# Kernel tuning notes

Hardware: AMD Instinct MI355X
Metric: run time of the kernel (lower is better)

Reference implementation:

```python
import jax, jax.numpy as jnp
import numpy as np

N_NODES = 100000


def gcn_conv(x, src, dst, W, b, n_nodes):
    """PyG GCNConv: add self-loops, symmetric degree normalization, X W, scatter-add."""
    # Linear transform first (small out dim -> cheaper messages)
    h = x @ W  # [N, F_out]
    # Add self-loops
    loop = jnp.arange(n_nodes, dtype=src.dtype)
    s = jnp.concatenate([src, loop])
    d = jnp.concatenate([dst, loop])
    # Degree (in-degree over dst, incl. self-loops), deg^{-1/2}
    deg = jax.ops.segment_sum(jnp.ones_like(d, dtype=h.dtype), d, num_segments=n_nodes)
    dinv = jnp.where(deg > 0, jax.lax.rsqrt(deg), 0.0)
    norm = dinv[s] * dinv[d]  # [E+N]
    # Gather-scale-scatter aggregation
    msgs = h[s] * norm[:, None]  # [E+N, F_out]
    out = jax.ops.segment_sum(msgs, d, num_segments=n_nodes)
    return out + b


def setup_inputs() -> dict:
    key = jax.random.key(0)
    ks = jax.random.split(key, 4)
    n, f_in, f_hid, f_out = N_NODES, 512, 16, 7
    n_edges = 3200000
    x = jax.random.normal(ks[0], (n, f_in), dtype=jnp.float32)
    edge_index = jax.random.randint(ks[1], (2, n_edges), 0, n, dtype=jnp.int64)
    W1 = jax.random.normal(ks[2], (f_in, f_hid), dtype=jnp.float32) / np.sqrt(f_in)
    b1 = jnp.zeros((f_hid,), dtype=jnp.float32)
    W2 = jax.random.normal(ks[3], (f_hid, f_out), dtype=jnp.float32) / np.sqrt(f_hid)
    b2 = jnp.zeros((f_out,), dtype=jnp.float32)
    return {"x": x, "edge_index": edge_index, "W1": W1, "b1": b1, "W2": W2, "b2": b2}


def reference(x, edge_index, W1, b1, W2, b2):
    n = x.shape[0]
    src, dst = edge_index[0], edge_index[1]
    h = gcn_conv(x, src, dst, W1, b1, n)
    h = jax.nn.relu(h)
    out = gcn_conv(h, src, dst, W2, b2, n)
    return out
```

## Files before the change

kernel.cpp:

```cpp
#include <hip/hip_runtime.h>

#define F_IN 512
#define F_HID 16
#define F_OUT 7
#define BUCKET 128
#define LB 7
#define CHUNK 4096
#define MAXNB 1024
#define BSTR 8192
#define BSTR2 8704

#define RPB 256
#define KHALF 256

typedef int   int4v   __attribute__((ext_vector_type(4)));
typedef float float2v __attribute__((ext_vector_type(2)));
typedef float float4v __attribute__((ext_vector_type(4)));
typedef unsigned int uint4v __attribute__((ext_vector_type(4)));

static __device__ __forceinline__ unsigned short f2bf(float f) {
    unsigned int u = __float_as_uint(f);
    u += 0x7FFFu + ((u >> 16) & 1u);
    return (unsigned short)(u >> 16);
}
static __device__ __forceinline__ float bf2f(unsigned short s) {
    return __uint_as_float((unsigned int)s << 16);
}

__global__ void k_init(int* __restrict__ cursor, int NB) {
    int i = blockIdx.x * 256 + threadIdx.x;
    if (i < NB) cursor[i] = i * BSTR;
}

__global__ __launch_bounds__(256) void k_place4(
        const int* __restrict__ src, const int* __restrict__ dst,
        int* __restrict__ cursor, int* __restrict__ bedges, int E, int NB) {
    __shared__ int h[MAXNB];
    __shared__ int s[MAXNB];
    __shared__ int wtot[4];
    __shared__ int sedge[CHUNK];
    __shared__ unsigned short sbkt[CHUNK];
    int t = threadIdx.x, blk = blockIdx.x;
    for (int i = t; i < MAXNB; i += 256) h[i] = 0;
    __syncthreads();
    int base = blk * CHUNK;
    int4v d4[4], s4[4];
#pragma unroll
    for (int it = 0; it < 4; ++it) {
        int e = base + (it * 256 + t) * 4;
        if (e < E) {
            d4[it] = __builtin_nontemporal_load((const int4v*)(dst + e));
            s4[it] = __builtin_nontemporal_load((const int4v*)(src + e));
        } else {
            int sent = NB << LB;
            d4[it].x = sent; d4[it].y = sent; d4[it].z = sent; d4[it].w = sent;
            s4[it].x = 0;    s4[it].y = 0;    s4[it].z = 0;    s4[it].w = 0;
        }
        atomicAdd(&h[d4[it].x >> LB], 1);
        atomicAdd(&h[d4[it].y >> LB], 1);
        atomicAdd(&h[d4[it].z >> LB], 1);
        atomicAdd(&h[d4[it].w >> LB], 1);
    }
    __syncthreads();
    int i0 = t << 2;
    int v0 = h[i0], v1 = h[i0 + 1], v2 = h[i0 + 2], v3 = h[i0 + 3];
    int sum = v0 + v1 + v2 + v3;
    int lane = t & 63, w = t >> 6;
    int sincl = sum;
#pragma unroll
    for (int off = 1; off < 64; off <<= 1) {
        int u = __shfl_up(sincl, off);
        if (lane >= off) sincl += u;
    }
    if (lane == 63) wtot[w] = sincl;
    __syncthreads();
    int wb = 0;
#pragma unroll
    for (int ww = 0; ww < 4; ++ww) if (ww < w) wb += wtot[ww];
    int excl = wb + sincl - sum;
    int pe[4] = {excl, excl + v0, excl + v0 + v1, excl + v0 + v1 + v2};
    int vv[4] = {v0, v1, v2, v3};
#pragma unroll
    for (int j = 0; j < 4; ++j) {
        int i = i0 + j;
        h[i] = pe[j];
        int db = 0;
        if (i < NB && vv[j] > 0)
            db = atomicAdd(&cursor[i], vv[j]) - pe[j];
        s[i] = db;
    }
    __syncthreads();
#pragma unroll
    for (int it = 0; it < 4; ++it) {
        int d, sv, b, p;
        d = d4[it].x; sv = s4[it].x; b = d >> LB; p = atomicAdd(&h[b], 1);
        sedge[p] = (sv << 8) | (d & (BUCKET - 1)); sbkt[p] = (unsigned short)b;
        d = d4[it].y; sv = s4[it].y; b = d >> LB; p = atomicAdd(&h[b], 1);
        sedge[p] = (sv << 8) | (d & (BUCKET - 1)); sbkt[p] = (unsigned short)b;
        d = d4[it].z; sv = s4[it].z; b = d >> LB; p = atomicAdd(&h[b], 1);
        sedge[p] = (sv << 8) | (d & (BUCKET - 1)); sbkt[p] = (unsigned short)b;
        d = d4[it].w; sv = s4[it].w; b = d >> LB; p = atomicAdd(&h[b], 1);
        sedge[p] = (sv << 8) | (d & (BUCKET - 1)); sbkt[p] = (unsigned short)b;
    }
    __syncthreads();
    for (int j = t; j < CHUNK; j += 256) {
        int b = sbkt[j];
        if (b < NB)
            __builtin_nontemporal_store(sedge[j], bedges + s[b] + j);
    }
}

__global__ __launch_bounds__(256) void k_psort(
        const int* __restrict__ cursor, const int* __restrict__ bedges,
        int* __restrict__ bedges2, float* __restrict__ dinv,
        int* __restrict__ node_off, int* __restrict__ node_nq, int n) {
    __shared__ int cnt[BUCKET];
    __shared__ int sc[BUCKET];
    __shared__ int cur[BUCKET];
    __shared__ int sedge[BSTR2];
    int b = blockIdx.x, t = threadIdx.x;
    int base = b * BSTR;
    int ne = cursor[b] - base;
    if (t < BUCKET) cnt[t] = 0;
    __syncthreads();
    int nq = ne >> 2, tail = ne & 3;
    for (int q = t; q < nq; q += 256) {
        int4v v = *(const int4v*)(bedges + base + (q << 2));
        atomicAdd(&cnt[v.x & 127], 1);
        atomicAdd(&cnt[v.y & 127], 1);
        atomicAdd(&cnt[v.z & 127], 1);
        atomicAdd(&cnt[v.w & 127], 1);
    }
    if (t < tail) atomicAdd(&cnt[bedges[base + (nq << 2) + t] & 127], 1);
    __syncthreads();
    int p = 0;
    if (t < BUCKET) { p = (cnt[t] + 3) & ~3; sc[t] = p; }
    __syncthreads();
    for (int off = 1; off < BUCKET; off <<= 1) {
        int v = 0;
        if (t < BUCKET) { v = sc[t]; if (t >= off) v += sc[t - off]; }
        __syncthreads();
        if (t < BUCKET) sc[t] = v;
        __syncthreads();
    }
    if (t < BUCKET) {
        int w = sc[t] - p;
        cur[t] = w;
        int node = b * BUCKET + t;
        if (node < n) {
            dinv[node] = rsqrtf((float)(cnt[t] + 1));
            node_off[node] = b * BSTR2 + w;
            node_nq[node] = p >> 2;
        }
    }
    __syncthreads();
    for (int q = t; q < nq; q += 256) {
        int4v v = *(const int4v*)(bedges + base + (q << 2));
        int pos;
        pos = atomicAdd(&cur[v.x & 127], 1); sedge[pos] = v.x >> 8;
        pos = atomicAdd(&cur[v.y & 127], 1); sedge[pos] = v.y >> 8;
        pos = atomicAdd(&cur[v.z & 127], 1); sedge[pos] = v.z >> 8;
        pos = atomicAdd(&cur[v.w & 127], 1); sedge[pos] = v.w >> 8;
    }
    if (t < tail) {
        int v = bedges[base + (nq << 2) + t];
        int pos = atomicAdd(&cur[v & 127], 1); sedge[pos] = v >> 8;
    }
    __syncthreads();
    if (t < BUCKET) {
        int endc = cur[t];
        for (int i = endc; i < sc[t]; ++i) sedge[i] = n;
    }
    __syncthreads();
    int total = sc[BUCKET - 1];
    int* dst2 = bedges2 + b * BSTR2;
    for (int j4 = t; j4 < (total >> 2); j4 += 256) {
        int4v v = *(const int4v*)(sedge + (j4 << 2));
        __builtin_nontemporal_store(v, (int4v*)(dst2 + (j4 << 2)));
    }
}

__global__ __launch_bounds__(256) void k_gemm1d(
        const float* __restrict__ x, const float* __restrict__ W,
        float* __restrict__ part, int n) {
    int b  = blockIdx.x >> 1;
    int ks = blockIdx.x & 1;
    int r  = b * RPB + threadIdx.x;
    if (r >= n) return;
    const float* xr = x + (size_t)r * F_IN + ks * KHALF;
    const float2v* W2v = (const float2v*)(W + (size_t)ks * KHALF * F_HID);

    float2v acc2[F_HID / 2];
#pragma unroll
    for (int c = 0; c < F_HID / 2; ++c) acc2[c] = (float2v){0.0f, 0.0f};

    for (int k4 = 0; k4 < KHALF / 4; k4 += 8) {
        float4v v[8];
#pragma unroll
        for (int j = 0; j < 8; ++j)
            v[j] = *(const float4v*)(xr + ((k4 + j) << 2));
#pragma unroll
        for (int j = 0; j < 8; ++j) {
            int k = (k4 + j) << 2;
#pragma unroll
            for (int c2 = 0; c2 < F_HID / 2; ++c2) {
                acc2[c2] += v[j].x * W2v[(k + 0) * (F_HID / 2) + c2];
                acc2[c2] += v[j].y * W2v[(k + 1) * (F_HID / 2) + c2];
                acc2[c2] += v[j].z * W2v[(k + 2) * (F_HID / 2) + c2];
                acc2[c2] += v[j].w * W2v[(k + 3) * (F_HID / 2) + c2];
            }
        }
    }
    const float* a = (const float*)acc2;
    float4v* o = (float4v*)(part + ((size_t)ks * n + r) * F_HID);
    float4v w0 = {a[0],  a[1],  a[2],  a[3]};
    float4v w1 = {a[4],  a[5],  a[6],  a[7]};
    float4v w2 = {a[8],  a[9],  a[10], a[11]};
    float4v w3 = {a[12], a[13], a[14], a[15]};
    o[0] = w0; o[1] = w1; o[2] = w2; o[3] = w3;
}

__global__ void k_fin1(const float* __restrict__ part, const float* __restrict__ dinv,
                       unsigned short* __restrict__ h1b, unsigned short* __restrict__ h2b,
                       int n) {
    int tg = blockIdx.x * 256 + threadIdx.x;
    int r = tg >> 4, c = tg & 15;
    if (r > n) return;
    if (r == n) {
        h1b[(size_t)r * F_HID + c] = 0;
        if (c < 8) h2b[((size_t)r << 3) + c] = 0;
        return;
    }
    float v = part[(size_t)r * F_HID + c] + part[((size_t)n + r) * F_HID + c];
    h1b[(size_t)r * F_HID + c] = f2bf(dinv[r] * v);
}

__global__ __launch_bounds__(1024) void k_aggF1(
        const int* __restrict__ node_off, const int* __restrict__ node_nq,
        const int* __restrict__ bedges2, const unsigned short* __restrict__ h1b,
        const float* __restrict__ dinv, const float* __restrict__ b1,
        const float* __restrict__ W2, unsigned short* __restrict__ h2b, int n) {
    int tg = blockIdx.x * 1024 + threadIdx.x;
    int node = tg >> 4, c = tg & 15;
    if (node >= n) return;
    int off = node_off[node], nq = node_nq[node];
    float acc = bf2f(h1b[(size_t)node * F_HID + c]);
    for (int q = 0; q < nq; ++q) {
        int4v s = *(const int4v*)(bedges2 + off + (q << 2));
        float v0 = bf2f(h1b[(size_t)s.x * F_HID + c]);
        float v1 = bf2f(h1b[(size_t)s.y * F_HID + c]);
        float v2 = bf2f(h1b[(size_t)s.z * F_HID + c]);
        float v3 = bf2f(h1b[(size_t)s.w * F_HID + c]);
        acc += v0 + v1 + v2 + v3;
    }
    float dv = dinv[node];
    float z = fmaxf(dv * acc + b1[c], 0.0f);
    float h[F_OUT];
#pragma unroll
    for (int o = 0; o < F_OUT; ++o) h[o] = z * W2[c * F_OUT + o];
#pragma unroll
    for (int sft = 8; sft >= 1; sft >>= 1)
#pragma unroll
        for (int o = 0; o < F_OUT; ++o) h[o] += __shfl_xor(h[o], sft, 16);
    if (c < 8) {
        unsigned short w = (c < F_OUT) ? f2bf(dv * h[c]) : (unsigned short)0;
        h2b[((size_t)node << 3) + c] = w;
    }
}

__global__ __launch_bounds__(1024) void k_aggF2(
        const int* __restrict__ node_off, const int* __restrict__ node_nq,
        const int* __restrict__ bedges2, const unsigned short* __restrict__ h2b,
        const float* __restrict__ dinv, const float* __restrict__ b2,
        float* __restrict__ out, int n) {
    int tg = blockIdx.x * 1024 + threadIdx.x;
    int node = tg >> 3, c = tg & 7;
    if (node >= n) return;
    int off = node_off[node], nq = node_nq[node];
    float acc = bf2f(h2b[((size_t)node << 3) + c]);
    for (int q = 0; q < nq; ++q) {
        int4v s = *(const int4v*)(bedges2 + off + (q << 2));
        float v0 = bf2f(h2b[((size_t)s.x << 3) + c]);
        float v1 = bf2f(h2b[((size_t)s.y << 3) + c]);
        float v2 = bf2f(h2b[((size_t)s.z << 3) + c]);
        float v3 = bf2f(h2b[((size_t)s.w << 3) + c]);
        acc += v0 + v1 + v2 + v3;
    }
    if (c < F_OUT)
        out[(size_t)node * F_OUT + c] = dinv[node] * acc + b2[c];
}

extern "C" void kernel_launch(void* const* d_in, const int* in_sizes, int n_in,
                              void* d_out, int out_size, void* d_ws, size_t ws_size,
                              hipStream_t stream) {
    const float* x  = (const float*)d_in[0];
    const int*   ei = (const int*)d_in[1];
    const float* W1 = (const float*)d_in[2];
    const float* b1 = (const float*)d_in[3];
    const float* W2 = (const float*)d_in[4];
    const float* b2 = (const float*)d_in[5];
    float* out = (float*)d_out;

    const int n = in_sizes[0] / F_IN;
    const int E = in_sizes[1] / 2;
    const int* src = ei;
    const int* dst = ei + E;

    const int NB = (n + BUCKET - 1) / BUCKET;
    const int PBLK = (E + CHUNK - 1) / CHUNK;

    size_t Np = ((size_t)n + 3) & ~(size_t)3;
    char* ws = (char*)d_ws;
    int*   cursor       = (int*)ws;             ws += MAXNB * 4;
    float* dinv         = (float*)ws;           ws += Np * 4;
    int*   node_off     = (int*)ws;             ws += Np * 4;
    int*   node_nq      = (int*)ws;             ws += Np * 4;
    int*   bedges       = (int*)ws;             ws += (size_t)NB * BSTR * 4;
    int*   bedges2      = (int*)ws;             ws += (size_t)NB * BSTR2 * 4;
    unsigned short* h1b = (unsigned short*)ws;  ws += (Np + 4) * F_HID * 2;
    unsigned short* h2b = (unsigned short*)ws;  ws += (Np + 4) * 8 * 2;
    float* part         = (float*)bedges;

    k_init   <<<(NB + 255) / 256, 256, 0, stream>>>(cursor, NB);
    k_place4 <<<PBLK, 256, 0, stream>>>(src, dst, cursor, bedges, E, NB);
    k_psort  <<<NB, 256, 0, stream>>>(cursor, bedges, bedges2, dinv, node_off, node_nq, n);
    k_gemm1d <<<((n + RPB - 1) / RPB) * 2, 256, 0, stream>>>(x, W1, part, n);
    k_fin1   <<<((n + 1) * 16 + 255) / 256, 256, 0, stream>>>(part, dinv, h1b, h2b, n);
    k_aggF1  <<<((size_t)n * 16 + 1023) / 1024, 1024, 0, stream>>>(node_off, node_nq, bedges2, h1b, dinv, b1, W2, h2b, n);
    k_aggF2  <<<((size_t)n * 8 + 1023) / 1024, 1024, 0, stream>>>(node_off, node_nq, bedges2, h2b, dinv, b2, out, n);
}
```

Before: 472.0 us.

## Stage X tiles through double-buffered LDS with coalesced loads in first GEMM

The first-layer X·W1 kernel used to have each thread stream its own 2 KB row slice, so global loads across a wavefront were strided by a full row. It now has groups of four threads load contiguous 64-byte pieces of each row into a padded, double-buffered shared-memory tile. The next 16-column chunk is prefetched into registers while the current one is computed. This aims for coalesced loads and overlap of memory with FMAs. The cost is a barrier per 16-column step and extra LDS traffic, in a kernel that is likely bound by global memory bandwidth.

```diff
diff --git a/kernel.cpp b/kernel.cpp
--- a/kernel.cpp
+++ b/kernel.cpp
@@ -12,6 +12,8 @@
 
 #define RPB 256
 #define KHALF 256
+#define KC2 16
+#define LSTR2 17
 
 typedef int   int4v   __attribute__((ext_vector_type(4)));
 typedef float float2v __attribute__((ext_vector_type(2)));
@@ -180,44 +182,82 @@
     }
 }
 
-__global__ __launch_bounds__(256) void k_gemm1d(
+__global__ __launch_bounds__(256) void k_gemm1db(
         const float* __restrict__ x, const float* __restrict__ W,
         float* __restrict__ part, int n) {
+    __shared__ float xs[2][RPB * LSTR2];
     int b  = blockIdx.x >> 1;
     int ks = blockIdx.x & 1;
-    int r  = b * RPB + threadIdx.x;
-    if (r >= n) return;
-    const float* xr = x + (size_t)r * F_IN + ks * KHALF;
-    const float2v* W2v = (const float2v*)(W + (size_t)ks * KHALF * F_HID);
+    int r0 = b * RPB;
+    int t  = threadIdx.x;
+    int r  = r0 + t;
+    int kbase = ks * KHALF;
 
     float2v acc2[F_HID / 2];
 #pragma unroll
     for (int c = 0; c < F_HID / 2; ++c) acc2[c] = (float2v){0.0f, 0.0f};
 
-    for (int k4 = 0; k4 < KHALF / 4; k4 += 8) {
-        float4v v[8];
-#pragma unroll
-        for (int j = 0; j < 8; ++j)
-            v[j] = *(const float4v*)(xr + ((k4 + j) << 2));
-#pragma unroll
-        for (int j = 0; j < 8; ++j) {
-            int k = (k4 + j) << 2;
-#pragma unroll
-            for (int c2 = 0; c2 < F_HID / 2; ++c2) {
-                acc2[c2] += v[j].x * W2v[(k + 0) * (F_HID / 2) + c2];
-                acc2[c2] += v[j].y * W2v[(k + 1) * (F_HID / 2) + c2];
-                acc2[c2] += v[j].z * W2v[(k + 2) * (F_HID / 2) + c2];
-                acc2[c2] += v[j].w * W2v[(k + 3) * (F_HID / 2) + c2];
+    int lr = t >> 2;
+    int c4 = t & 3;
+
+    float4v pv[4];
+#pragma unroll
+    for (int j = 0; j < 4; ++j) {
+        int gr = r0 + j * 64 + lr;
+        float4v v = {0.0f, 0.0f, 0.0f, 0.0f};
+        if (gr < n)
+            v = *(const float4v*)(x + (size_t)gr * F_IN + kbase + c4 * 4);
+        pv[j] = v;
+    }
+#pragma unroll
+    for (int j = 0; j < 4; ++j) {
+        float* d = xs[0] + (j * 64 + lr) * LSTR2 + c4 * 4;
+        d[0] = pv[j].x; d[1] = pv[j].y; d[2] = pv[j].z; d[3] = pv[j].w;
+    }
+    __syncthreads();
+
+    int cur = 0;
+    for (int kc = 0; kc < KHALF; kc += KC2) {
+        if (kc + KC2 < KHALF) {
+#pragma unroll
+            for (int j = 0; j < 4; ++j) {
+                int gr = r0 + j * 64 + lr;
+                float4v v = {0.0f, 0.0f, 0.0f, 0.0f};
+                if (gr < n)
+                    v = *(const float4v*)(x + (size_t)gr * F_IN + kbase + kc + KC2 + c4 * 4);
+                pv[j] = v;
             }
         }
-    }
-    const float* a = (const float*)acc2;
-    float4v* o = (float4v*)(part + ((size_t)ks * n + r) * F_HID);
-    float4v w0 = {a[0],  a[1],  a[2],  a[3]};
-    float4v w1 = {a[4],  a[5],  a[6],  a[7]};
-    float4v w2 = {a[8],  a[9],  a[10], a[11]};
-    float4v w3 = {a[12], a[13], a[14], a[15]};
-    o[0] = w0; o[1] = w1; o[2] = w2; o[3] = w3;
+        if (r < n) {
+            const float* xrow = xs[cur] + t * LSTR2;
+            const float2v* Wk2 = (const float2v*)(W + (size_t)(kbase + kc) * F_HID);
+#pragma unroll
+            for (int k = 0; k < KC2; ++k) {
+                float xv = xrow[k];
+#pragma unroll
+                for (int c2 = 0; c2 < F_HID / 2; ++c2)
+                    acc2[c2] += xv * Wk2[k * (F_HID / 2) + c2];
+            }
+        }
+        if (kc + KC2 < KHALF) {
+#pragma unroll
+            for (int j = 0; j < 4; ++j) {
+                float* d = xs[cur ^ 1] + (j * 64 + lr) * LSTR2 + c4 * 4;
+                d[0] = pv[j].x; d[1] = pv[j].y; d[2] = pv[j].z; d[3] = pv[j].w;
+            }
+        }
+        __syncthreads();
+        cur ^= 1;
+    }
+    if (r < n) {
+        const float* a = (const float*)acc2;
+        float4v* o = (float4v*)(part + ((size_t)ks * n + r) * F_HID);
+        float4v w0 = {a[0],  a[1],  a[2],  a[3]};
+        float4v w1 = {a[4],  a[5],  a[6],  a[7]};
+        float4v w2 = {a[8],  a[9],  a[10], a[11]};
+        float4v w3 = {a[12], a[13], a[14], a[15]};
+        o[0] = w0; o[1] = w1; o[2] = w2; o[3] = w3;
+    }
 }
 
 __global__ void k_fin1(const float* __restrict__ part, const float* __restrict__ dinv,
@@ -321,11 +361,11 @@
     unsigned short* h2b = (unsigned short*)ws;  ws += (Np + 4) * 8 * 2;
     float* part         = (float*)bedges;
 
-    k_init   <<<(NB + 255) / 256, 256, 0, stream>>>(cursor, NB);
-    k_place4 <<<PBLK, 256, 0, stream>>>(src, dst, cursor, bedges, E, NB);
-    k_psort  <<<NB, 256, 0, stream>>>(cursor, bedges, bedges2, dinv, node_off, node_nq, n);
-    k_gemm1d <<<((n + RPB - 1) / RPB) * 2, 256, 0, stream>>>(x, W1, part, n);
-    k_fin1   <<<((n + 1) * 16 + 255) / 256, 256, 0, stream>>>(part, dinv, h1b, h2b, n);
-    k_aggF1  <<<((size_t)n * 16 + 1023) / 1024, 1024, 0, stream>>>(node_off, node_nq, bedges2, h1b, dinv, b1, W2, h2b, n);
-    k_aggF2  <<<((size_t)n * 8 + 1023) / 1024, 1024, 0, stream>>>(node_off, node_nq, bedges2, h2b, dinv, b2, out, n);
-}
+    k_init    <<<(NB + 255) / 256, 256, 0, stream>>>(cursor, NB);
+    k_place4  <<<PBLK, 256, 0, stream>>>(src, dst, cursor, bedges, E, NB);
+    k_psort   <<<NB, 256, 0, stream>>>(cursor, bedges, bedges2, dinv, node_off, node_nq, n);
+    k_gemm1db <<<((n + RPB - 1) / RPB) * 2, 256, 0, stream>>>(x, W1, part, n);
+    k_fin1    <<<((n + 1) * 16 + 255) / 256, 256, 0, stream>>>(part, dinv, h1b, h2b, n);
+    k_aggF1   <<<((size_t)n * 16 + 1023) / 1024, 1024, 0, stream>>>(node_off, node_nq, bedges2, h1b, dinv, b1, W2, h2b, n);
+    k_aggF2   <<<((size_t)n * 8 + 1023) / 1024, 1024, 0, stream>>>(node_off, node_nq, bedges2, h2b, dinv, b2, out, n);
+}
```

Result: slower. 521.9 us (+10.6%).
